# Kernel optimization log

Hardware: AMD Instinct MI355X
Metric: run time of the kernel (lower is better)

Reference implementation:

```python
import jax, jax.numpy as jnp
import numpy as np

B, L = 8, 1024
VOCAB = 5000
DW = 256            # d_word_vec = d_model
H = 3 * DW          # hidden_size = 768
NH, HD = 12, 64     # n_head, d_k
D = NH * HD         # 768 = nhead*head_dim
D_INNER = 3072
N_LAYERS = 2
N_HIDDEN = 1024
N_OUT = 5000
MASK = 0
SCALE = 1.0 / float(np.sqrt(HD))


def _sinusoid(n_pos, d_hid):
    pos = np.arange(n_pos, dtype=np.float64)[:, None]
    hid = np.arange(d_hid)[None, :]
    tab = pos / np.power(10000.0, 2 * (hid // 2) / d_hid)
    tab[:, 0::2] = np.sin(tab[:, 0::2])
    tab[:, 1::2] = np.cos(tab[:, 1::2])
    tab[0] = 0.0  # padding_idx=0
    return jnp.asarray(tab, dtype=jnp.float32)


def _ln(x, g, b, eps=1e-5):
    mu = x.mean(-1, keepdims=True)
    var = ((x - mu) ** 2).mean(-1, keepdims=True)
    return (x - mu) * jax.lax.rsqrt(var + eps) * g + b


def _dense(x, w, b):
    # w: [out, in] (torch Conv 1x1 / Linear convention)
    return jnp.einsum('...i,oi->...o', x, w) + b


def _pwff(x, w1, b1, w2, b2, g, bn):
    out = _dense(jax.nn.relu(_dense(x, w1, b1)), w2, b2)
    return _ln(out + x, g, bn)


def _msa1(x, relay, wq, bq, wk, bk, wv, bv, wo, bo):
    # x: [B, L, H] nodes, relay: [B, H]. Star-Transformer ring attention:
    # window = 3 local neighbors + the relay node (4 keys per query).
    Bx, Lx, _ = x.shape
    q = _dense(x, wq, bq).reshape(Bx, Lx, NH, HD)
    k = _dense(x, wk, bk).reshape(Bx, Lx, NH, HD)
    v = _dense(x, wv, bv).reshape(Bx, Lx, NH, HD)
    kp = jnp.pad(k, ((0, 0), (1, 1), (0, 0), (0, 0)))
    vp = jnp.pad(v, ((0, 0), (1, 1), (0, 0), (0, 0)))
    k_win = jnp.stack([kp[:, u:u + Lx] for u in range(3)], axis=2)  # [B,L,3,NH,HD]
    v_win = jnp.stack([vp[:, u:u + Lx] for u in range(3)], axis=2)
    rk = _dense(relay, wk, bk).reshape(Bx, NH, HD)
    rv = _dense(relay, wv, bv).reshape(Bx, NH, HD)
    s_loc = jnp.einsum('blnh,blwnh->blwn', q, k_win)
    s_rel = jnp.einsum('blnh,bnh->bln', q, rk)
    scores = jnp.concatenate([s_loc, s_rel[:, :, None, :]], axis=2) * SCALE  # [B,L,4,NH]
    a = jax.nn.softmax(scores, axis=2)
    att = jnp.einsum('blwn,blwnh->blnh', a[:, :, :3], v_win) + a[:, :, 3][..., None] * rv[:, None]
    return _dense(att.reshape(Bx, Lx, D), wo, bo)


def _msa2(relay, nodes, smask, wq, bq, wk, bk, wv, bv, wo, bo):
    # Satellite->planet global attention: single query (relay) over [relay; nodes].
    Bx = relay.shape[0]
    y = jnp.concatenate([relay[:, None, :], nodes], axis=1)  # [B, 1+L, H]
    q = _dense(relay, wq, bq).reshape(Bx, NH, HD)
    k = _dense(y, wk, bk).reshape(Bx, -1, NH, HD)
    v = _dense(y, wv, bv).reshape(Bx, -1, NH, HD)
    pre = jnp.einsum('bnh,bsnh->bns', q, k) * SCALE
    pre = jnp.where(smask[:, None, :], -jnp.inf, pre)
    a = jax.nn.softmax(pre, axis=2)
    att = jnp.einsum('bns,bsnh->bnh', a, v).reshape(Bx, D)
    return _dense(att, wo, bo)


def setup_inputs():
    ks = iter(jax.random.split(jax.random.key(0), 40))
    def w(shape):
        return jax.random.normal(next(ks), shape, dtype=jnp.float32) * 0.02
    def z(shape):
        return jnp.zeros(shape, jnp.float32)
    def o(shape):
        return jnp.ones(shape, jnp.float32)
    inp = {}
    inp['src_seq'] = jax.random.randint(next(ks), (B, L, 3), 0, VOCAB, dtype=jnp.int32)
    inp['positions'] = jax.random.randint(next(ks), (B,), 0, L, dtype=jnp.int32)
    inp['emb'] = w((VOCAB, DW))
    inp['pos_table'] = _sinusoid(L, H)
    inp['norm_g'] = o((N_LAYERS, H)); inp['norm_b'] = z((N_LAYERS, H))
    inp['pw_w1'] = w((N_LAYERS, D_INNER, H)); inp['pw_b1'] = z((N_LAYERS, D_INNER))
    inp['pw_w2'] = w((N_LAYERS, H, D_INNER)); inp['pw_b2'] = z((N_LAYERS, H))
    inp['pw_g'] = o((N_LAYERS, H)); inp['pw_bn'] = z((N_LAYERS, H))
    for p in ['ring', 'star']:
        inp[p + '_wq'] = w((N_LAYERS, D, H)); inp[p + '_bq'] = z((N_LAYERS, D))
        inp[p + '_wk'] = w((N_LAYERS, D, H)); inp[p + '_bk'] = z((N_LAYERS, D))
        inp[p + '_wv'] = w((N_LAYERS, D, H)); inp[p + '_bv'] = z((N_LAYERS, D))
        inp[p + '_wo'] = w((N_LAYERS, H, D)); inp[p + '_bo'] = z((N_LAYERS, H))
    inp['head_w1'] = w((3, N_HIDDEN, 2 * H)); inp['head_b1'] = z((3, N_HIDDEN))
    inp['head_w2'] = w((3, N_OUT, N_HIDDEN)); inp['head_b2'] = z((3, N_OUT))
    return inp


def reference(src_seq, positions, emb, pos_table, norm_g, norm_b, pw_w1, pw_b1, pw_w2, pw_b2, pw_g, pw_bn, ring_wq, ring_bq, ring_wk, ring_bk, ring_wv, ring_bv, ring_wo, ring_bo, star_wq, star_bq, star_wk, star_bk, star_wv, star_bv, star_wo, star_bo, head_w1, head_b1, head_w2, head_b2):
    Bx, Lx, _ = src_seq.shape
    # [B,L,3,DW] -> [B,L,H], add (frozen) sinusoid positional encoding
    x = emb[src_seq].reshape(Bx, Lx, H) + pos_table[None, :Lx]
    mask_pad = src_seq[:, :, 0] == MASK               # True at padded positions
    smask = jnp.concatenate([jnp.zeros((Bx, 1), bool), mask_pad], axis=1)
    nodes = x
    relay = x.mean(axis=1)                            # [B, H]
    for i in range(N_LAYERS):
        h = _pwff(nodes, pw_w1[i], pw_b1[i], pw_w2[i], pw_b2[i], pw_g[i], pw_bn[i])
        ring = _msa1(h, relay, ring_wq[i], ring_bq[i], ring_wk[i], ring_bk[i], ring_wv[i], ring_bv[i], ring_wo[i], ring_bo[i])
        nodes = jax.nn.leaky_relu(_ln(ring, norm_g[i], norm_b[i]))
        relay = jax.nn.leaky_relu(_msa2(relay, nodes, smask, star_wq[i], star_bq[i], star_wk[i], star_bk[i], star_wv[i], star_bv[i], star_wo[i], star_bo[i]))
        nodes = jnp.where(mask_pad[:, :, None], 0.0, nodes)
    target = nodes[jnp.arange(Bx), positions]         # [B, H]
    ft = jnp.concatenate([relay, target], axis=1)     # [B, 2H]
    outs = [_dense(jax.nn.relu(_dense(ft, head_w1[j], head_b1[j])), head_w2[j], head_b2[j]) for j in range(3)]
    return jnp.concatenate(outs, axis=1).reshape(3 * Bx, N_OUT)
```

## Files before the change

### kernel.cpp

```cpp
#include <hip/hip_runtime.h>
#include <cstdint>
#include <cstddef>


typedef unsigned short u16;
typedef __attribute__((ext_vector_type(4))) float f32x4;
typedef __attribute__((ext_vector_type(8))) __bf16 bf16x8;

#define NB 8
#define SEQ 1024
#define HDIM 768
#define NHEAD 12
#define HD 64
#define DINNER 3072
#define NHID 1024
#define NOUT 5000
#define ATT_SCALE 0.125f

static __device__ __forceinline__ float b2f(u16 u) {
  union { float f; uint32_t i; } v; v.i = ((uint32_t)u) << 16; return v.f;
}
static __device__ __forceinline__ u16 f2b(float f) {
  union { float f; uint32_t i; } v; v.f = f;
  uint32_t r = v.i + 0x7fffu + ((v.i >> 16) & 1u);
  return (u16)(r >> 16);
}
static __device__ __forceinline__ float2 b2f2(uint32_t u) {
  union { float f; uint32_t i; } lo, hi;
  lo.i = u << 16; hi.i = u & 0xffff0000u;
  return make_float2(lo.f, hi.f);
}

static __device__ __forceinline__ void gl2lds16(const void* g, void* l) {
  __builtin_amdgcn_global_load_lds(
      (__attribute__((address_space(1))) void*)(uintptr_t)g,
      (__attribute__((address_space(3))) void*)l, 16, 0, 0);
}

static __device__ __forceinline__ float blk_sum(float v, float* red) {
  #pragma unroll
  for (int off = 32; off > 0; off >>= 1) v += __shfl_down(v, off, 64);
  if ((threadIdx.x & 63) == 0) red[threadIdx.x >> 6] = v;
  __syncthreads();
  float r = red[0] + red[1] + red[2] + red[3];
  __syncthreads();
  return r;
}
static __device__ __forceinline__ float blk_max(float v, float* red) {
  #pragma unroll
  for (int off = 32; off > 0; off >>= 1) v = fmaxf(v, __shfl_down(v, off, 64));
  if ((threadIdx.x & 63) == 0) red[threadIdx.x >> 6] = v;
  __syncthreads();
  float r = fmaxf(fmaxf(red[0], red[1]), fmaxf(red[2], red[3]));
  __syncthreads();
  return r;
}

struct Cvt4 {
  const float* s0; const float* s1; const float* s2; const float* s3;
  u16* d0; u16* d1; u16* d2; u16* d3;
  int c1, c2, c3, c4;
};
__global__ __launch_bounds__(256) void cvt4_k(Cvt4 a) {
  const int i = blockIdx.x * 256 + threadIdx.x;
  if (i >= a.c4) return;
  const float* s; u16* d; int j;
  if (i < a.c1)      { s = a.s0; d = a.d0; j = i; }
  else if (i < a.c2) { s = a.s1; d = a.d1; j = i - a.c1; }
  else if (i < a.c3) { s = a.s2; d = a.d2; j = i - a.c2; }
  else               { s = a.s3; d = a.d3; j = i - a.c3; }
  const float4 v = ((const float4*)s)[j];
  ushort4 o;
  o.x = f2b(v.x); o.y = f2b(v.y); o.z = f2b(v.z); o.w = f2b(v.w);
  ((ushort4*)d)[j] = o;
}

template <int ACT, int TM>
__global__ __launch_bounds__(256) void gemm_bt(
    const u16* __restrict__ A,
    const u16* W0, const u16* W1, const u16* W2,
    const float* b0, const float* b1, const float* b2,
    u16* C0, u16* C1, u16* C2,
    int M, int N, int K) {
  constexpr int MI = TM / 32;
  __shared__ u16 As[TM * 32];
  __shared__ u16 Bs[128 * 32];
  const int z = blockIdx.z;
  const u16* W = z == 0 ? W0 : (z == 1 ? W1 : W2);
  const float* bias = z == 0 ? b0 : (z == 1 ? b1 : b2);
  u16* C = z == 0 ? C0 : (z == 1 ? C1 : C2);

  const int tid  = threadIdx.x;
  const int wave = tid >> 6;
  const int lane = tid & 63;
  const int bm = blockIdx.y * TM;
  const int bn = blockIdx.x * 128;
  const int wrq = wave >> 1, wcq = wave & 1;
  const int r16 = lane & 15, quad = lane >> 4;
  const int srow = lane >> 2;
  const int scol = (lane & 3) << 3;

  f32x4 acc[MI][4] = {};

  for (int k0 = 0; k0 < K; k0 += 32) {
    __syncthreads();
    #pragma unroll
    for (int t = 0; t < TM / 64; ++t) {
      const int rowa = wave * (TM / 4) + t * 16;
      gl2lds16(A + (size_t)(bm + rowa + srow) * K + (k0 + scol), (char*)As + (rowa << 6));
    }
    #pragma unroll
    for (int t = 0; t < 2; ++t) {
      const int rowb = wave * 32 + t * 16;
      gl2lds16(W + (size_t)(bn + rowb + srow) * K + (k0 + scol), (char*)Bs + (rowb << 6));
    }
    __syncthreads();
    bf16x8 af[MI], bf[4];
    #pragma unroll
    for (int i = 0; i < MI; ++i)
      af[i] = *reinterpret_cast<const bf16x8*>(&As[(wrq * (TM / 2) + i * 16 + r16) * 32 + quad * 8]);
    #pragma unroll
    for (int j = 0; j < 4; ++j)
      bf[j] = *reinterpret_cast<const bf16x8*>(&Bs[(wcq * 64 + j * 16 + r16) * 32 + quad * 8]);
    #pragma unroll
    for (int i = 0; i < MI; ++i)
      #pragma unroll
      for (int j = 0; j < 4; ++j)
        acc[i][j] = __builtin_amdgcn_mfma_f32_16x16x32_bf16(af[i], bf[j], acc[i][j], 0, 0, 0);
  }

  #pragma unroll
  for (int j = 0; j < 4; ++j) {
    const int n = bn + wcq * 64 + j * 16 + r16;
    const float bv = bias[n];
    #pragma unroll
    for (int i = 0; i < MI; ++i) {
      const int m0 = bm + wrq * (TM / 2) + i * 16 + quad * 4;
      #pragma unroll
      for (int r = 0; r < 4; ++r) {
        float vv = acc[i][j][r] + bv;
        if (ACT == 1) vv = fmaxf(vv, 0.0f);
        C[(size_t)(m0 + r) * N + n] = f2b(vv);
      }
    }
  }
}

__global__ __launch_bounds__(256) void embed_k(
    const int* __restrict__ src, const float* __restrict__ emb,
    const float* __restrict__ pt, float* __restrict__ x,
    u16* __restrict__ xb) {
  const int r = blockIdx.x;
  const int l = r & (SEQ - 1);
  const int tid = threadIdx.x;
  #pragma unroll
  for (int it = 0; it < 3; ++it) {
    const int idx = tid + it * 256;
    const int c = idx >> 8, d = idx & 255;
    const int tok = src[r * 3 + c];
    const float v = emb[(size_t)tok * 256 + d] + pt[(size_t)l * HDIM + idx];
    x[(size_t)r * HDIM + idx] = v;
    xb[(size_t)r * HDIM + idx] = f2b(v);
  }
}

__global__ __launch_bounds__(256) void relay_mean1_k(
    const float* __restrict__ x, float* __restrict__ part) {
  const int cg = blockIdx.x, seg = blockIdx.y, b = blockIdx.z;
  const int h = cg * 256 + threadIdx.x;
  float s = 0.f;
  const int l0 = seg * 64;
  for (int l = l0; l < l0 + 64; ++l) s += x[((size_t)b * SEQ + l) * HDIM + h];
  part[((size_t)b * 16 + seg) * HDIM + h] = s;
}
__global__ __launch_bounds__(256) void relay_mean2_k(
    const float* __restrict__ part, float* __restrict__ relay) {
  const int b = blockIdx.y;
  const int h = blockIdx.x * 256 + threadIdx.x;
  float s = 0.f;
  #pragma unroll
  for (int i = 0; i < 16; ++i) s += part[((size_t)b * 16 + i) * HDIM + h];
  relay[b * HDIM + h] = s * (1.0f / 1024.0f);
}

__global__ __launch_bounds__(256) void ln_resid_k(
    const u16* __restrict__ pre, const float* __restrict__ res,
    const float* __restrict__ g, const float* __restrict__ bb,
    u16* __restrict__ out) {
  __shared__ float red[4];
  const int r = blockIdx.x;
  const int tid = threadIdx.x;
  const size_t base = (size_t)r * HDIM;
  float v0 = b2f(pre[base + tid])       + res[base + tid];
  float v1 = b2f(pre[base + tid + 256]) + res[base + tid + 256];
  float v2 = b2f(pre[base + tid + 512]) + res[base + tid + 512];
  const float mu = blk_sum(v0 + v1 + v2, red) * (1.0f / 768.0f);
  v0 -= mu; v1 -= mu; v2 -= mu;
  const float var = blk_sum(v0 * v0 + v1 * v1 + v2 * v2, red) * (1.0f / 768.0f);
  const float rs = rsqrtf(var + 1e-5f);
  out[base + tid]       = f2b(v0 * rs * g[tid]       + bb[tid]);
  out[base + tid + 256] = f2b(v1 * rs * g[tid + 256] + bb[tid + 256]);
  out[base + tid + 512] = f2b(v2 * rs * g[tid + 512] + bb[tid + 512]);
}

__global__ __launch_bounds__(256) void ln_leaky_mask_k(
    const u16* __restrict__ pre, const float* __restrict__ g,
    const float* __restrict__ bb, const int* __restrict__ src,
    float* __restrict__ out, u16* __restrict__ outb) {
  __shared__ float red[4];
  const int r = blockIdx.x;
  const int tid = threadIdx.x;
  const size_t base = (size_t)r * HDIM;
  float v0 = b2f(pre[base + tid]);
  float v1 = b2f(pre[base + tid + 256]);
  float v2 = b2f(pre[base + tid + 512]);
  const float mu = blk_sum(v0 + v1 + v2, red) * (1.0f / 768.0f);
  v0 -= mu; v1 -= mu; v2 -= mu;
  const float var = blk_sum(v0 * v0 + v1 * v1 + v2 * v2, red) * (1.0f / 768.0f);
  const float rs = rsqrtf(var + 1e-5f);
  const bool masked = (src[r * 3] == 0);
  float y0 = v0 * rs * g[tid]       + bb[tid];
  float y1 = v1 * rs * g[tid + 256] + bb[tid + 256];
  float y2 = v2 * rs * g[tid + 512] + bb[tid + 512];
  y0 = y0 > 0.f ? y0 : 0.01f * y0;
  y1 = y1 > 0.f ? y1 : 0.01f * y1;
  y2 = y2 > 0.f ? y2 : 0.01f * y2;
  if (masked) { y0 = 0.f; y1 = 0.f; y2 = 0.f; }
  out[base + tid]       = y0;  outb[base + tid]       = f2b(y0);
  out[base + tid + 256] = y1;  outb[base + tid + 256] = f2b(y1);
  out[base + tid + 512] = y2;  outb[base + tid + 512] = f2b(y2);
}

__global__ __launch_bounds__(256) void ring_attn_k(
    const u16* __restrict__ q, const u16* __restrict__ k,
    const u16* __restrict__ v, const float* __restrict__ rk,
    const float* __restrict__ rv, u16* __restrict__ att) {
  __shared__ float qs[HDIM];
  __shared__ float aw[NHEAD][4];
  const int r = blockIdx.x;
  const int b = r >> 10, l = r & (SEQ - 1);
  const int tid = threadIdx.x;
  const size_t base = (size_t)r * HDIM;
  #pragma unroll
  for (int it = 0; it < 3; ++it) {
    const int idx = tid + it * 256;
    qs[idx] = b2f(q[base + idx]);
  }
  __syncthreads();
  if (tid < 192) {
    const int u_ = tid >> 2;
    const int l4 = tid & 3;
    const int n = u_ >> 2, w = u_ & 3;
    const float* qrow = qs + n * HD + l4 * 16;
    float a = 0.f;
    if (w < 3) {
      const int ll = l - 1 + w;
      if (ll >= 0 && ll < SEQ) {
        const uint4* kp4 =
            (const uint4*)(k + base + (size_t)(w - 1) * HDIM + n * HD + l4 * 16);
        #pragma unroll
        for (int t = 0; t < 2; ++t) {
          const uint4 u = kp4[t];
          const float2 f0 = b2f2(u.x), f1 = b2f2(u.y);
          const float2 f2_ = b2f2(u.z), f3 = b2f2(u.w);
          const float* q8 = qrow + t * 8;
          a += q8[0] * f0.x + q8[1] * f0.y + q8[2] * f1.x + q8[3] * f1.y
             + q8[4] * f2_.x + q8[5] * f2_.y + q8[6] * f3.x + q8[7] * f3.y;
        }
      }
    } else {
      const float4* kp4 = (const float4*)(rk + b * HDIM + n * HD + l4 * 16);
      #pragma unroll
      for (int t = 0; t < 4; ++t) {
        const float4 kv = kp4[t];
        const float* q4 = qrow + t * 4;
        a += q4[0] * kv.x + q4[1] * kv.y + q4[2] * kv.z + q4[3] * kv.w;
      }
    }
    a += __shfl_xor(a, 1, 4);
    a += __shfl_xor(a, 2, 4);
    if (l4 == 0) aw[n][w] = a * ATT_SCALE;
  }
  __syncthreads();
  if (tid < NHEAD) {
    const float s0 = aw[tid][0], s1 = aw[tid][1], s2 = aw[tid][2], s3 = aw[tid][3];
    const float m = fmaxf(fmaxf(s0, s1), fmaxf(s2, s3));
    const float e0 = __expf(s0 - m), e1 = __expf(s1 - m);
    const float e2 = __expf(s2 - m), e3 = __expf(s3 - m);
    const float inv = 1.0f / (e0 + e1 + e2 + e3);
    aw[tid][0] = e0 * inv; aw[tid][1] = e1 * inv;
    aw[tid][2] = e2 * inv; aw[tid][3] = e3 * inv;
  }
  __syncthreads();
  #pragma unroll
  for (int it = 0; it < 3; ++it) {
    const int idx = tid + it * 256;
    const int n = idx >> 6;
    float acc = aw[n][3] * rv[b * HDIM + idx];
    if (l > 0)       acc += aw[n][0] * b2f(v[base - HDIM + idx]);
    acc += aw[n][1] * b2f(v[base + idx]);
    if (l < SEQ - 1) acc += aw[n][2] * b2f(v[base + HDIM + idx]);
    att[base + idx] = f2b(acc);
  }
}

__global__ __launch_bounds__(256) void msa2_attn_k(
    const float* __restrict__ q2, const float* __restrict__ rk2,
    const float* __restrict__ rv2, const u16* __restrict__ k2,
    const u16* __restrict__ v2, const int* __restrict__ src,
    float* __restrict__ att) {
  __shared__ float qs[HD];
  __shared__ float sc[SEQ + 1];
  __shared__ float red[4];
  __shared__ float vred[4][HD];
  const int bid = blockIdx.x;
  const int b = bid / NHEAD, n = bid % NHEAD;
  const int tid = threadIdx.x;
  const int hb = b * HDIM + n * HD;
  if (tid < HD) qs[tid] = q2[hb + tid];
  __syncthreads();
  float lmax = -1e30f;
  for (int s = tid; s <= SEQ; s += 256) {
    float sco;
    if (s == 0) {
      float a = 0.f;
      #pragma unroll
      for (int d = 0; d < HD; ++d) a += qs[d] * rk2[hb + d];
      sco = a * ATT_SCALE;
    } else {
      const int l = s - 1;
      if (src[(b * SEQ + l) * 3] == 0) {
        sco = -1e30f;
      } else {
        const uint4* kp4 =
            (const uint4*)(k2 + ((size_t)b * SEQ + l) * HDIM + n * HD);
        float a = 0.f;
        #pragma unroll
        for (int t = 0; t < 8; ++t) {
          const uint4 u = kp4[t];
          const float2 f0 = b2f2(u.x), f1 = b2f2(u.y);
          const float2 f2_ = b2f2(u.z), f3 = b2f2(u.w);
          const float* q8 = qs + t * 8;
          a += q8[0] * f0.x + q8[1] * f0.y + q8[2] * f1.x + q8[3] * f1.y
             + q8[4] * f2_.x + q8[5] * f2_.y + q8[6] * f3.x + q8[7] * f3.y;
        }
        sco = a * ATT_SCALE;
      }
    }
    sc[s] = sco;
    lmax = fmaxf(lmax, sco);
  }
  lmax = blk_max(lmax, red);
  float lsum = 0.f;
  for (int s = tid; s <= SEQ; s += 256) {
    const float e = __expf(sc[s] - lmax);
    sc[s] = e;
    lsum += e;
  }
  lsum = blk_sum(lsum, red);
  {
    const int dd = tid & 63, grp = tid >> 6;
    float acc = 0.f;
    const u16* vp = v2 + (size_t)b * SEQ * HDIM + n * HD + dd;
    for (int l = grp; l < SEQ; l += 4)
      acc += sc[l + 1] * b2f(vp[(size_t)l * HDIM]);
    vred[grp][dd] = acc;
  }
  __syncthreads();
  if (tid < HD) {
    const float inv = 1.0f / lsum;
    const float a = sc[0] * rv2[hb + tid]
                  + vred[0][tid] + vred[1][tid] + vred[2][tid] + vred[3][tid];
    att[hb + tid] = a * inv;
  }
}

__global__ __launch_bounds__(256) void relay_proj_k(
    const float* __restrict__ A, int N, int nm,
    const float* W0, const float* W1, const float* W2,
    const float* b0, const float* b1, const float* b2v,
    float* O0, float* O1, float* O2, int act) {
  const int wid = blockIdx.x * 4 + (threadIdx.x >> 6);
  const int lane = threadIdx.x & 63;
  const int mat = wid / N, n = wid % N;
  const float* W  = mat == 0 ? W0 : (mat == 1 ? W1 : W2);
  const float* bb = mat == 0 ? b0 : (mat == 1 ? b1 : b2v);
  float* O        = mat == 0 ? O0 : (mat == 1 ? O1 : O2);
  const float4* wr = (const float4*)(W + (size_t)n * HDIM);
  float acc[NB] = {};
  #pragma unroll
  for (int it = 0; it < 3; ++it) {
    const int k4 = it * 64 + lane;
    const float4 wv = wr[k4];
    #pragma unroll
    for (int b = 0; b < NB; ++b) {
      const float4 av = *(const float4*)&A[b * HDIM + k4 * 4];
      acc[b] += av.x * wv.x + av.y * wv.y + av.z * wv.z + av.w * wv.w;
    }
  }
  #pragma unroll
  for (int b = 0; b < NB; ++b) {
    float a = acc[b];
    #pragma unroll
    for (int off = 32; off > 0; off >>= 1) a += __shfl_down(a, off, 64);
    if (lane == 0) {
      float v = a + bb[n];
      if (act == 2) v = v > 0.f ? v : 0.01f * v;
      O[(size_t)b * N + n] = v;
    }
  }
}

__global__ __launch_bounds__(256) void ft_k(
    const float* __restrict__ relay, const float* __restrict__ nodes,
    const int* __restrict__ positions, float* __restrict__ ft) {
  const int gid = blockIdx.x * 256 + threadIdx.x;
  const int b = gid / 1536, j = gid % 1536;
  if (j < HDIM) {
    ft[gid] = relay[b * HDIM + j];
  } else {
    const int p = positions[b];
    ft[gid] = nodes[((size_t)b * SEQ + p) * HDIM + (j - HDIM)];
  }
}

__global__ __launch_bounds__(256) void head1_k(
    const float* __restrict__ ft, const float* __restrict__ w,
    const float* __restrict__ bias, float* __restrict__ hid) {
  __shared__ float fs[NB * 1536];
  const int j = blockIdx.y;
  {
    const float4* s4 = (const float4*)ft;
    float4* d4 = (float4*)fs;
    for (int i = threadIdx.x; i < (NB * 1536) / 4; i += 256) d4[i] = s4[i];
  }
  __syncthreads();
  const int wave = threadIdx.x >> 6, lane = threadIdx.x & 63;
  const int o = blockIdx.x * 4 + wave;
  const float4* wr = (const float4*)(w + ((size_t)j * NHID + o) * 1536);
  float acc[NB] = {};
  #pragma unroll
  for (int it = 0; it < 6; ++it) {
    const int k4 = it * 64 + lane;
    const float4 wv = wr[k4];
    #pragma unroll
    for (int b = 0; b < NB; ++b) {
      const float4 hv = *(const float4*)&fs[b * 1536 + k4 * 4];
      acc[b] += hv.x * wv.x + hv.y * wv.y + hv.z * wv.z + hv.w * wv.w;
    }
  }
  #pragma unroll
  for (int b = 0; b < NB; ++b) {
    float a = acc[b];
    #pragma unroll
    for (int off = 32; off > 0; off >>= 1) a += __shfl_down(a, off, 64);
    if (lane == 0)
      hid[((size_t)j * NB + b) * NHID + o] = fmaxf(a + bias[j * NHID + o], 0.f);
  }
}

__global__ __launch_bounds__(256) void head2_k(
    const float* __restrict__ hid, const float* __restrict__ w,
    const float* __restrict__ bias, float* __restrict__ out) {
  __shared__ float hs[NB * NHID];
  const int j = blockIdx.y;
  {
    const float4* s4 = (const float4*)(hid + (size_t)j * NB * NHID);
    float4* d4 = (float4*)hs;
    for (int i = threadIdx.x; i < (NB * NHID) / 4; i += 256) d4[i] = s4[i];
  }
  __syncthreads();
  const int wave = threadIdx.x >> 6, lane = threadIdx.x & 63;
  const int o = blockIdx.x * 4 + wave;
  const float4* wr = (const float4*)(w + ((size_t)j * NOUT + o) * NHID);
  float acc[NB] = {};
  #pragma unroll
  for (int it = 0; it < 4; ++it) {
    const int k4 = it * 64 + lane;
    const float4 wv = wr[k4];
    #pragma unroll
    for (int b = 0; b < NB; ++b) {
      const float4 hv = *(const float4*)&hs[b * NHID + k4 * 4];
      acc[b] += hv.x * wv.x + hv.y * wv.y + hv.z * wv.z + hv.w * wv.w;
    }
  }
  #pragma unroll
  for (int b = 0; b < NB; ++b) {
    float a = acc[b];
    #pragma unroll
    for (int off = 32; off > 0; off >>= 1) a += __shfl_down(a, off, 64);
    if (lane == 0)
      out[(size_t)(b * 3 + j) * NOUT + o] = a + bias[j * NOUT + o];
  }
}

extern "C" void kernel_launch(void* const* d_in, const int* in_sizes, int n_in,
                              void* d_out, int out_size, void* d_ws, size_t ws_size,
                              hipStream_t stream) {
  (void)in_sizes; (void)n_in; (void)out_size; (void)ws_size;
  const int* src       = (const int*)d_in[0];
  const int* positions = (const int*)d_in[1];
  const float* emb   = (const float*)d_in[2];
  const float* pt    = (const float*)d_in[3];
  const float* norm_g = (const float*)d_in[4]; const float* norm_b = (const float*)d_in[5];
  const float* pw_w1 = (const float*)d_in[6];  const float* pw_b1 = (const float*)d_in[7];
  const float* pw_w2 = (const float*)d_in[8];  const float* pw_b2 = (const float*)d_in[9];
  const float* pw_g  = (const float*)d_in[10]; const float* pw_bn = (const float*)d_in[11];
  const float* ring_wq = (const float*)d_in[12]; const float* ring_bq = (const float*)d_in[13];
  const float* ring_wk = (const float*)d_in[14]; const float* ring_bk = (const float*)d_in[15];
  const float* ring_wv = (const float*)d_in[16]; const float* ring_bv = (const float*)d_in[17];
  const float* ring_wo = (const float*)d_in[18]; const float* ring_bo = (const float*)d_in[19];
  const float* star_wq = (const float*)d_in[20]; const float* star_bq = (const float*)d_in[21];
  const float* star_wk = (const float*)d_in[22]; const float* star_bk = (const float*)d_in[23];
  const float* star_wv = (const float*)d_in[24]; const float* star_bv = (const float*)d_in[25];
  const float* star_wo = (const float*)d_in[26]; const float* star_bo = (const float*)d_in[27];
  const float* head_w1 = (const float*)d_in[28]; const float* head_b1 = (const float*)d_in[29];
  const float* head_w2 = (const float*)d_in[30]; const float* head_b2 = (const float*)d_in[31];

  char* ws = (char*)d_ws;
  const size_t NTOK = (size_t)NB * SEQ * HDIM;
  float* nodes   = (float*)(ws);
  u16* preln     = (u16*)(ws + NTOK * 4);
  u16* cbase     = (u16*)(ws + NTOK * 6);
  u16* inner  = cbase;
  u16* slotC0 = cbase;
  u16* slotC1 = cbase + 1 * NTOK;
  u16* slotC2 = cbase + 2 * NTOK;
  u16* slotC3 = cbase + 3 * NTOK;
  u16* shared12  = (u16*)(ws + NTOK * 14);
  u16* wc        = (u16*)(ws + NTOK * 16);
  char* small    = ws + NTOK * 16 + 9437184;
  float* part  = (float*)(small);
  float* relay = (float*)(small + 393216);
  float* sb0 = (float*)(small + 393216 + 1 * 24576);
  float* sb1 = (float*)(small + 393216 + 2 * 24576);
  float* sb2 = (float*)(small + 393216 + 3 * 24576);
  float* sb3 = (float*)(small + 393216 + 4 * 24576);
  float* ftb = (float*)(small + 393216 + 5 * 24576);
  float* hid = (float*)(small + 393216 + 5 * 24576 + 49152);

  u16* nodes_b16 = shared12;
  u16* hbuf      = shared12;

  embed_k<<<NB * SEQ, 256, 0, stream>>>(src, emb, pt, nodes, nodes_b16);
  relay_mean1_k<<<dim3(3, 16, NB), 256, 0, stream>>>(nodes, part);
  relay_mean2_k<<<dim3(3, NB), 256, 0, stream>>>(part, relay);

  const int NW1 = DINNER * HDIM;
  const int NQK = HDIM * HDIM;

  for (int i = 0; i < 2; ++i) {
    const float* pw_w1_l = pw_w1 + (size_t)i * NW1;
    const float* pw_w2_l = pw_w2 + (size_t)i * NW1;
    const float* pw_b1_l = pw_b1 + (size_t)i * DINNER;
    const float* pw_b2_l = pw_b2 + (size_t)i * HDIM;
    const float* pw_g_l  = pw_g + (size_t)i * HDIM;
    const float* pw_bn_l = pw_bn + (size_t)i * HDIM;
    const float* ng_l = norm_g + (size_t)i * HDIM;
    const float* nb_l = norm_b + (size_t)i * HDIM;
    const float* rwq = ring_wq + (size_t)i * NQK; const float* rbq = ring_bq + (size_t)i * HDIM;
    const float* rwk = ring_wk + (size_t)i * NQK; const float* rbk = ring_bk + (size_t)i * HDIM;
    const float* rwv = ring_wv + (size_t)i * NQK; const float* rbv = ring_bv + (size_t)i * HDIM;
    const float* rwo = ring_wo + (size_t)i * NQK; const float* rbo = ring_bo + (size_t)i * HDIM;
    const float* swq = star_wq + (size_t)i * NQK; const float* sbq = star_bq + (size_t)i * HDIM;
    const float* swk = star_wk + (size_t)i * NQK; const float* sbk = star_bk + (size_t)i * HDIM;
    const float* swv = star_wv + (size_t)i * NQK; const float* sbv = star_bv + (size_t)i * HDIM;
    const float* swo = star_wo + (size_t)i * NQK; const float* sbo = star_bo + (size_t)i * HDIM;

    u16* wc_pw1 = wc;
    u16* wc_pw2 = wc + NW1;
    {
      Cvt4 a = { pw_w1_l, pw_w2_l, pw_w1_l, pw_w1_l,
                 wc_pw1, wc_pw2, wc_pw1, wc_pw1,
                 NW1 / 4, NW1 / 2, NW1 / 2, NW1 / 2 };
      cvt4_k<<<(NW1 / 2 + 255) / 256, 256, 0, stream>>>(a);
    }
    gemm_bt<1, 128><<<dim3(DINNER / 128, 64, 1), 256, 0, stream>>>(
        nodes_b16, wc_pw1, wc_pw1, wc_pw1, pw_b1_l, pw_b1_l, pw_b1_l,
        inner, inner, inner, NB * SEQ, DINNER, HDIM);
    gemm_bt<0, 64><<<dim3(HDIM / 128, 128, 1), 256, 0, stream>>>(
        inner, wc_pw2, wc_pw2, wc_pw2, pw_b2_l, pw_b2_l, pw_b2_l,
        preln, preln, preln, NB * SEQ, HDIM, DINNER);
    ln_resid_k<<<NB * SEQ, 256, 0, stream>>>(preln, nodes, pw_g_l, pw_bn_l, hbuf);

    u16* wc_rq = wc;
    u16* wc_rk = wc + NQK;
    u16* wc_rv = wc + 2 * NQK;
    u16* wc_ro = wc + 3 * NQK;
    {
      Cvt4 a = { rwq, rwk, rwv, rwo, wc_rq, wc_rk, wc_rv, wc_ro,
                 NQK / 4, NQK / 2, 3 * NQK / 4, NQK };
      cvt4_k<<<(NQK + 255) / 256, 256, 0, stream>>>(a);
    }
    gemm_bt<0, 64><<<dim3(HDIM / 128, 128, 3), 256, 0, stream>>>(
        hbuf, wc_rq, wc_rk, wc_rv, rbq, rbk, rbv,
        slotC0, slotC1, slotC2, NB * SEQ, HDIM, HDIM);
    relay_proj_k<<<2 * HDIM / 4, 256, 0, stream>>>(
        relay, HDIM, 2, rwk, rwv, rwk, rbk, rbv, rbk, sb0, sb1, sb2, 0);
    ring_attn_k<<<NB * SEQ, 256, 0, stream>>>(slotC0, slotC1, slotC2, sb0, sb1, slotC3);
    gemm_bt<0, 64><<<dim3(HDIM / 128, 128, 1), 256, 0, stream>>>(
        slotC3, wc_ro, wc_ro, wc_ro, rbo, rbo, rbo,
        preln, preln, preln, NB * SEQ, HDIM, HDIM);
    ln_leaky_mask_k<<<NB * SEQ, 256, 0, stream>>>(preln, ng_l, nb_l, src, nodes, nodes_b16);

    u16* wc_sk = wc;
    u16* wc_sv = wc + NQK;
    {
      Cvt4 a = { swk, swv, swk, swk, wc_sk, wc_sv, wc_sk, wc_sk,
                 NQK / 4, NQK / 2, NQK / 2, NQK / 2 };
      cvt4_k<<<(NQK / 2 + 255) / 256, 256, 0, stream>>>(a);
    }
    gemm_bt<0, 64><<<dim3(HDIM / 128, 128, 2), 256, 0, stream>>>(
        nodes_b16, wc_sk, wc_sv, wc_sv, sbk, sbv, sbv,
        slotC0, slotC1, slotC1, NB * SEQ, HDIM, HDIM);
    relay_proj_k<<<3 * HDIM / 4, 256, 0, stream>>>(
        relay, HDIM, 3, swq, swk, swv, sbq, sbk, sbv, sb0, sb1, sb2, 0);
    msa2_attn_k<<<NB * NHEAD, 256, 0, stream>>>(sb0, sb1, sb2, slotC0, slotC1, src, sb3);
    relay_proj_k<<<HDIM / 4, 256, 0, stream>>>(
        sb3, HDIM, 1, swo, swo, swo, sbo, sbo, sbo, relay, sb1, sb2, 2);
  }

  ft_k<<<48, 256, 0, stream>>>(relay, nodes, positions, ftb);
  head1_k<<<dim3(NHID / 4, 3), 256, 0, stream>>>(ftb, head_w1, head_b1, hid);
  head2_k<<<dim3(NOUT / 4, 3), 256, 0, stream>>>(hid, head_w2, head_b2, (float*)d_out);
}
```

Measured before the change: 1.090 ms.

## Multi-stage LDS pipeline with prefetch distance two in GEMM kernel

```diff
diff --git a/kernel.cpp b/kernel.cpp
--- a/kernel.cpp
+++ b/kernel.cpp
@@ -35,6 +35,15 @@
   __builtin_amdgcn_global_load_lds(
       (__attribute__((address_space(1))) void*)(uintptr_t)g,
       (__attribute__((address_space(3))) void*)l, 16, 0, 0);
+}
+
+template <int N>
+static __device__ __forceinline__ void wait_vmcnt() {
+  if constexpr (N == 0) asm volatile("s_waitcnt vmcnt(0)" ::: "memory");
+  else if constexpr (N == 3) asm volatile("s_waitcnt vmcnt(3)" ::: "memory");
+  else if constexpr (N == 4) asm volatile("s_waitcnt vmcnt(4)" ::: "memory");
+  else if constexpr (N == 6) asm volatile("s_waitcnt vmcnt(6)" ::: "memory");
+  else if constexpr (N == 8) asm volatile("s_waitcnt vmcnt(8)" ::: "memory");
 }
 
 static __device__ __forceinline__ float blk_sum(float v, float* red) {
@@ -83,8 +92,9 @@
     u16* C0, u16* C1, u16* C2,
     int M, int N, int K) {
   constexpr int MI = TM / 32;
-  __shared__ u16 As[TM * 32];
-  __shared__ u16 Bs[128 * 32];
+  constexpr int S = TM / 64 + 2;
+  __shared__ u16 As[4][TM * 32];
+  __shared__ u16 Bs[4][128 * 32];
   const int z = blockIdx.z;
   const u16* W = z == 0 ? W0 : (z == 1 ? W1 : W2);
   const float* bias = z == 0 ? b0 : (z == 1 ? b1 : b2);
@@ -102,26 +112,51 @@
 
   f32x4 acc[MI][4] = {};
 
-  for (int k0 = 0; k0 < K; k0 += 32) {
-    __syncthreads();
-    #pragma unroll
-    for (int t = 0; t < TM / 64; ++t) {
-      const int rowa = wave * (TM / 4) + t * 16;
-      gl2lds16(A + (size_t)(bm + rowa + srow) * K + (k0 + scol), (char*)As + (rowa << 6));
-    }
-    #pragma unroll
-    for (int t = 0; t < 2; ++t) {
-      const int rowb = wave * 32 + t * 16;
-      gl2lds16(W + (size_t)(bn + rowb + srow) * K + (k0 + scol), (char*)Bs + (rowb << 6));
-    }
-    __syncthreads();
+  const int nk = K >> 5;
+
+  auto STAGE = [&](int s, int t) {
+    const int k0 = t << 5;
+    #pragma unroll
+    for (int q = 0; q < TM / 64; ++q) {
+      const int rowa = wave * (TM / 4) + q * 16;
+      gl2lds16(A + (size_t)(bm + rowa + srow) * K + (k0 + scol),
+               (char*)&As[s][0] + (rowa << 6));
+    }
+    #pragma unroll
+    for (int q = 0; q < 2; ++q) {
+      const int rowb = wave * 32 + q * 16;
+      gl2lds16(W + (size_t)(bn + rowb + srow) * K + (k0 + scol),
+               (char*)&Bs[s][0] + (rowb << 6));
+    }
+  };
+
+  STAGE(0, 0);
+  if (1 < nk) STAGE(1, 1);
+
+  for (int t = 0; t < nk; ++t) {
+    const int s = t & 3;
+    if (t + 2 < nk) {
+      STAGE((t + 2) & 3, t + 2);
+      __builtin_amdgcn_sched_barrier(0);
+      wait_vmcnt<2 * S>();
+    } else if (t + 1 < nk) {
+      wait_vmcnt<S>();
+    } else {
+      wait_vmcnt<0>();
+    }
+    __builtin_amdgcn_sched_barrier(0);
+    __builtin_amdgcn_s_barrier();
+    __builtin_amdgcn_sched_barrier(0);
+
     bf16x8 af[MI], bf[4];
     #pragma unroll
     for (int i = 0; i < MI; ++i)
-      af[i] = *reinterpret_cast<const bf16x8*>(&As[(wrq * (TM / 2) + i * 16 + r16) * 32 + quad * 8]);
+      af[i] = *reinterpret_cast<const bf16x8*>(
+          &As[s][(wrq * (TM / 2) + i * 16 + r16) * 32 + quad * 8]);
     #pragma unroll
     for (int j = 0; j < 4; ++j)
-      bf[j] = *reinterpret_cast<const bf16x8*>(&Bs[(wcq * 64 + j * 16 + r16) * 32 + quad * 8]);
+      bf[j] = *reinterpret_cast<const bf16x8*>(
+          &Bs[s][(wcq * 64 + j * 16 + r16) * 32 + quad * 8]);
     #pragma unroll
     for (int i = 0; i < MI; ++i)
       #pragma unroll
```

New measurement: 1.087 ms. No clear change (-0.3%).
